# Kernel tuning notes

Measured on AMD Instinct MI355X. Metric: run time of the kernel, lower is better.

The kernel has to match this reference:

```python
import jax, jax.numpy as jnp
import numpy as np

C = 256      # all_channel
HW = 60      # all_dim
D = HW * HW  # 3600 spatial tokens
B = 1        # batch (torch loop returns only the last sample)
ROUNDS = 5   # propagate_layers


def _attention(ex, q, W_lin, W_gate):
    # ex, q: [B,C,H,W]
    b = ex.shape[0]
    exf = ex.reshape(b, C, D)            # [b,C,D]
    qf = q.reshape(b, C, D)              # [b,C,D]
    # linear_e on exemplar tokens: y = x @ W^T  (torch Linear, no bias)
    corr = jnp.einsum('bdc,ec->bde', exf.transpose(0, 2, 1), W_lin)  # [b,D,C]
    A = jnp.einsum('bdc,bcj->bdj', corr, qf)  # [b,D,D] affinity
    # torch: B = softmax(A^T, dim=1); att = bmm(qf, B)
    # equivalent: att[b,c,i] = sum_j softmax_j(A[b,i,:])[j] * qf[b,c,j]
    P = jax.nn.softmax(A, axis=-1)            # [b,D,D]
    att = jnp.einsum('bij,bcj->bci', P, qf).reshape(b, C, HW, HW)
    # 1x1 conv gate (out channels = 1, no bias) + sigmoid
    mask = jax.nn.sigmoid(jnp.einsum('c,bchw->bhw', W_gate, att))[:, None]
    return att * mask


def _conv3x3(x, W, b):
    y = jax.lax.conv_general_dilated(
        x, W, window_strides=(1, 1), padding='SAME',
        dimension_numbers=('NCHW', 'OIHW', 'NCHW'))
    return y + b[None, :, None, None]


def _conv1x1(x, W, b):
    return jnp.einsum('oi,bihw->bohw', W, x) + b[None, :, None, None]


def _convgru(inp, prev, Wr, br, Wu, bu, Wo, bo):
    st = jnp.concatenate([inp, prev], axis=1)                 # [b,2C,H,W]
    u = jax.nn.sigmoid(_conv1x1(st, Wu, bu))                  # update gate
    r = jax.nn.sigmoid(_conv1x1(st, Wr, br))                  # reset gate
    o = jnp.tanh(_conv1x1(jnp.concatenate([inp, prev * r], axis=1), Wo, bo))
    return prev * (1.0 - u) + o * u


def setup_inputs() -> dict:
    key = jax.random.key(0)
    ks = jax.random.split(key, 10)
    f32 = jnp.float32
    g = lambda k, shape, s: jax.random.normal(k, shape, dtype=f32) * s
    return {
        'infeature1': jax.random.normal(ks[0], (B, C, HW, HW), f32),
        'infeature2': jax.random.normal(ks[1], (B, C, HW, HW), f32),
        'infeature3': jax.random.normal(ks[2], (B, C, HW, HW), f32),
        'W_lin': g(ks[3], (C, C), 0.02),          # linear_e weight [out,in]
        'W_gate': g(ks[4], (C,), 0.01),           # gate 1x1 conv (out=1)
        'W_cf': g(ks[5], (C, 2 * C, 3, 3), 0.01), # conv_fusion OIHW
        'b_cf': jnp.zeros((C,), f32),
        'W_reset': g(ks[6], (C, 2 * C), 0.02), 'b_reset': jnp.zeros((C,), f32),
        'W_update': g(ks[7], (C, 2 * C), 0.02), 'b_update': jnp.zeros((C,), f32),
        'W_out': g(ks[8], (C, 2 * C), 0.02), 'b_out': jnp.zeros((C,), f32),
    }


def reference(infeature1, infeature2, infeature3, W_lin, W_gate, W_cf, b_cf,
              W_reset, b_reset, W_update, b_update, W_out, b_out):
    ex, q, q1 = infeature1, infeature2, infeature3
    for _ in range(ROUNDS):
        a1 = _conv3x3(jnp.concatenate([_attention(ex, q, W_lin, W_gate),
                                       _attention(ex, q1, W_lin, W_gate)], 1), W_cf, b_cf)
        a2 = _conv3x3(jnp.concatenate([_attention(q, ex, W_lin, W_gate),
                                       _attention(q, q1, W_lin, W_gate)], 1), W_cf, b_cf)
        a3 = _conv3x3(jnp.concatenate([_attention(q1, ex, W_lin, W_gate),
                                       _attention(q1, q, W_lin, W_gate)], 1), W_cf, b_cf)
        h1 = _convgru(a1, ex, W_reset, b_reset, W_update, b_update, W_out, b_out)
        h2 = _convgru(a2, q, W_reset, b_reset, W_update, b_update, W_out, b_out)
        h3 = _convgru(a3, q1, W_reset, b_reset, W_update, b_update, W_out, b_out)
        ex, q, q1 = h1, h2, h3
    # torch forward returns the exemplar/query/query1 of the LAST batch sample
    return (ex[-1:], q[-1:], q1[-1:])
```

## Files before the change

kernel.cpp:

```cpp
#include <hip/hip_runtime.h>

typedef float f32x4_t __attribute__((ext_vector_type(4)));
typedef short bf16x8_t __attribute__((ext_vector_type(8)));

#define MFMA16(A,B,C) __builtin_amdgcn_mfma_f32_16x16x32_bf16((A),(B),(C),0,0,0)

static constexpr int CC = 256;
static constexpr int NP = 3600;
static constexpr int PP = 3648;
static constexpr int CPOS = 3906;

static constexpr size_t SZ_F  = (size_t)PP*CC*4;
static constexpr size_t SZ_H  = (size_t)PP*CC*2;
static constexpr size_t SZ_CV = (size_t)CPOS*512*2;

static constexpr size_t O_SF   = 0;
static constexpr size_t O_STH  = O_SF   + 3*SZ_F;
static constexpr size_t O_STL  = O_STH  + 3*SZ_H;
static constexpr size_t O_SCH  = O_STL  + 3*SZ_H;
static constexpr size_t O_SCL  = O_SCH  + 3*SZ_H;
static constexpr size_t O_CORH = O_SCL  + 3*SZ_H;
static constexpr size_t O_CORL = O_CORH + 3*SZ_H;
static constexpr size_t O_CVH  = O_CORL + 3*SZ_H;
static constexpr size_t O_CVL  = O_CVH  + 3*SZ_CV;
static constexpr size_t O_WLH  = O_CVL  + 3*SZ_CV;
static constexpr size_t O_WLL  = O_WLH  + 131072;
static constexpr size_t O_WURH = O_WLL  + 131072;
static constexpr size_t O_WURL = O_WURH + 524288;
static constexpr size_t O_WOH  = O_WURL + 524288;
static constexpr size_t O_WOL  = O_WOH  + 262144;
static constexpr size_t O_WKH  = O_WOL  + 262144;
static constexpr size_t O_WKL  = O_WKH  + 2359296;
static constexpr size_t O_X    = O_WKL  + 2359296;
static constexpr size_t O_PML  = O_X;
static constexpr size_t O_PO   = O_X + 1048576;
static constexpr size_t O_AH   = O_X;
static constexpr size_t O_AL   = O_AH + 3*SZ_H;
static constexpr size_t O_U    = O_AL + 3*SZ_H;
static constexpr size_t O_PRH  = O_U  + 3*SZ_F;
static constexpr size_t O_PRL  = O_PRH + 3*SZ_H;

#define WSPTR(T, OFF) ((T*)(ws + (OFF)))

__device__ __forceinline__ unsigned short f2bf(float f){
  unsigned u = __builtin_bit_cast(unsigned, f);
  u += 0x7FFFu + ((u >> 16) & 1u);
  return (unsigned short)(u >> 16);
}
__device__ __forceinline__ float bf2f(unsigned short h){
  unsigned u = ((unsigned)h) << 16;
  return __builtin_bit_cast(float, u);
}
__device__ __forceinline__ void split_bf(float x, unsigned short &h, unsigned short &l){
  h = f2bf(x);
  l = f2bf(x - bf2f(h));
}

__device__ __forceinline__ void gll16(const void* g, void* l){
  __builtin_amdgcn_global_load_lds(
      (const __attribute__((address_space(1))) unsigned*)g,
      (__attribute__((address_space(3))) unsigned*)l, 16, 0, 0);
}

__device__ __forceinline__ void stage64(unsigned short* dst, const unsigned short* __restrict__ src, int ld){
  int t = threadIdx.x, r0 = t >> 3, c8 = (t & 7) * 8;
  #pragma unroll
  for(int h = 0; h < 2; h++){
    int r = r0 + h*32;
    *(bf16x8_t*)&dst[r*72 + c8] = *(const bf16x8_t*)&src[(size_t)r*ld + c8];
  }
}

__device__ __forceinline__ void mfma64(const unsigned short* Ah, const unsigned short* Al,
                                       const unsigned short* Bh, const unsigned short* Bl,
                                       f32x4_t acc[4], int lane, int wid){
  int kb = (lane >> 4) * 8, lr = lane & 15;
  int arow = wid*16 + lr;
  #pragma unroll
  for(int kk = 0; kk < 2; kk++){
    bf16x8_t ah = *(const bf16x8_t*)&Ah[arow*72 + kk*32 + kb];
    bf16x8_t al = *(const bf16x8_t*)&Al[arow*72 + kk*32 + kb];
    #pragma unroll
    for(int ct = 0; ct < 4; ct++){
      int brow = ct*16 + lr;
      bf16x8_t bh = *(const bf16x8_t*)&Bh[brow*72 + kk*32 + kb];
      bf16x8_t bl = *(const bf16x8_t*)&Bl[brow*72 + kk*32 + kb];
      acc[ct] = MFMA16(ah, bh, acc[ct]);
      acc[ct] = MFMA16(ah, bl, acc[ct]);
      acc[ct] = MFMA16(al, bh, acc[ct]);
    }
  }
}

__global__ void k_zero(char* ws){
  size_t n = (6*SZ_CV)/16;
  uint4* p = (uint4*)(ws + O_CVH);
  uint4 z = {0,0,0,0};
  for(size_t x = (size_t)blockIdx.x*256 + threadIdx.x; x < n; x += (size_t)gridDim.x*256) p[x] = z;
}

__global__ void k_weights(char* ws, const float* __restrict__ Wlin, const float* __restrict__ Wup,
                          const float* __restrict__ Wrs, const float* __restrict__ Wo,
                          const float* __restrict__ Wcf){
  const size_t N1 = 65536, N2 = N1 + 262144, N3 = N2 + 131072, N4 = N3 + 1179648;
  for(size_t x = (size_t)blockIdx.x*256 + threadIdx.x; x < N4; x += (size_t)gridDim.x*256){
    float v; unsigned short *dh, *dl; size_t off;
    if(x < N1){
      v = Wlin[x]; dh = WSPTR(unsigned short, O_WLH); dl = WSPTR(unsigned short, O_WLL); off = x;
    } else if(x < N2){
      size_t i = x - N1; int e = (int)(i >> 9), c = (int)(i & 511);
      v = (e < 256) ? Wup[(size_t)e*512 + c] : Wrs[(size_t)(e-256)*512 + c];
      dh = WSPTR(unsigned short, O_WURH); dl = WSPTR(unsigned short, O_WURL); off = i;
    } else if(x < N3){
      size_t i = x - N2; v = Wo[i];
      dh = WSPTR(unsigned short, O_WOH); dl = WSPTR(unsigned short, O_WOL); off = i;
    } else {
      size_t i = x - N3; int t = (int)(i % 9); size_t rest = i / 9;
      int ic = (int)(rest & 511), o = (int)(rest >> 9);
      v = Wcf[i]; off = (size_t)t*131072 + (size_t)o*512 + ic;
      dh = WSPTR(unsigned short, O_WKH); dl = WSPTR(unsigned short, O_WKL);
    }
    unsigned short h, l; split_bf(v, h, l);
    dh[off] = h; dl[off] = l;
  }
}

__global__ __launch_bounds__(256) void k_transpose(char* ws, const float* __restrict__ in0,
                                                   const float* __restrict__ in1, const float* __restrict__ in2){
  __shared__ float tile[64*65];
  int z = blockIdx.z;
  const float* in = z == 0 ? in0 : (z == 1 ? in1 : in2);
  int p0 = blockIdx.x*64, c0 = blockIdx.y*64;
  float* sF = WSPTR(float, O_SF) + (size_t)z*PP*CC;
  unsigned short* sTh = WSPTR(unsigned short, O_STH) + (size_t)z*PP*CC;
  unsigned short* sTl = WSPTR(unsigned short, O_STL) + (size_t)z*PP*CC;
  unsigned short* sCh = WSPTR(unsigned short, O_SCH) + (size_t)z*PP*CC;
  unsigned short* sCl = WSPTR(unsigned short, O_SCL) + (size_t)z*PP*CC;
  int t = threadIdx.x, pl = t & 63, cq = t >> 6;
  #pragma unroll
  for(int rr = 0; rr < 16; rr++){
    int cl = rr*4 + cq, p = p0 + pl, c = c0 + cl;
    float v = (p < NP) ? in[(size_t)c*NP + p] : 0.f;
    tile[cl*65 + pl] = v;
    if(p < NP){
      unsigned short h, l; split_bf(v, h, l);
      sCh[(size_t)c*PP + p] = h; sCl[(size_t)c*PP + p] = l;
    }
  }
  __syncthreads();
  #pragma unroll
  for(int rr = 0; rr < 16; rr++){
    int prow = rr*4 + cq, p = p0 + prow, cl = pl;
    if(p < NP){
      float v = tile[cl*65 + prow];
      int c = c0 + cl;
      sF[(size_t)p*CC + c] = v;
      unsigned short h, l; split_bf(v, h, l);
      sTh[(size_t)p*CC + c] = h; sTl[(size_t)p*CC + c] = l;
    }
  }
}

__global__ __launch_bounds__(256,4) void k_corr(char* ws){
  __shared__ unsigned short Ah[64*72], Al[64*72], Bh[64*72], Bl[64*72];
  int z = blockIdx.z, m0 = blockIdx.x*64, n0 = blockIdx.y*64;
  const unsigned short* aH = WSPTR(const unsigned short, O_STH) + (size_t)z*PP*CC;
  const unsigned short* aL = WSPTR(const unsigned short, O_STL) + (size_t)z*PP*CC;
  const unsigned short* bH = WSPTR(const unsigned short, O_WLH);
  const unsigned short* bL = WSPTR(const unsigned short, O_WLL);
  unsigned short* cH = WSPTR(unsigned short, O_CORH) + (size_t)z*PP*CC;
  unsigned short* cL = WSPTR(unsigned short, O_CORL) + (size_t)z*PP*CC;
  int lane = threadIdx.x & 63, wid = threadIdx.x >> 6;
  f32x4_t acc[4] = {};
  for(int k0 = 0; k0 < 256; k0 += 64){
    __syncthreads();
    stage64(Ah, aH + (size_t)m0*256 + k0, 256);
    stage64(Al, aL + (size_t)m0*256 + k0, 256);
    stage64(Bh, bH + (size_t)n0*256 + k0, 256);
    stage64(Bl, bL + (size_t)n0*256 + k0, 256);
    __syncthreads();
    mfma64(Ah, Al, Bh, Bl, acc, lane, wid);
  }
  #pragma unroll
  for(int r = 0; r < 4; r++){
    int i = m0 + wid*16 + (lane >> 4)*4 + r;
    if(i >= NP) continue;
    #pragma unroll
    for(int ct = 0; ct < 4; ct++){
      int c = n0 + ct*16 + (lane & 15);
      unsigned short h, l; split_bf(acc[ct][r], h, l);
      cH[(size_t)i*CC + c] = h; cL[(size_t)i*CC + c] = l;
    }
  }
}

__global__ __launch_bounds__(256,2) void k_flash(char* ws, int nspl){
  __shared__ unsigned short KV[32768];
  __shared__ unsigned short PBh[4][1024], PBl[4][1024];
  int qt = blockIdx.x, pair = blockIdx.y, sp = blockIdx.z;
  int src = pair >> 1;
  int tgt = ((pair & 1) == 0) ? (src == 0 ? 1 : 0) : (src == 2 ? 1 : 2);
  const unsigned short* Qh = WSPTR(const unsigned short, O_CORH) + (size_t)src*PP*CC;
  const unsigned short* Ql = WSPTR(const unsigned short, O_CORL) + (size_t)src*PP*CC;
  const unsigned short* Kh = WSPTR(const unsigned short, O_STH)  + (size_t)tgt*PP*CC;
  const unsigned short* Kl = WSPTR(const unsigned short, O_STL)  + (size_t)tgt*PP*CC;
  const unsigned short* Vh = WSPTR(const unsigned short, O_SCH)  + (size_t)tgt*PP*CC;
  const unsigned short* Vl = WSPTR(const unsigned short, O_SCL)  + (size_t)tgt*PP*CC;
  int t = threadIdx.x, lane = t & 63, wid = t >> 6, lr = lane & 15, lk = lane >> 4;
  int rowi = lane >> 5, c_lds = lane & 31;
  int vrow8 = lane >> 3, vj = lane & 7;

  #pragma unroll
  for(int q = 0; q < 8; q++){
    int n = wid*8 + q;
    int row = 2*n + rowi;
    int gch = c_lds ^ (row & 7);
    size_t ga = (size_t)(qt*64 + row)*256 + gch*8;
    gll16(&Qh[ga], &KV[n*512]);
    gll16(&Ql[ga], &KV[16384 + n*512]);
  }
  asm volatile("s_waitcnt vmcnt(0)" ::: "memory");
  __syncthreads();
  bf16x8_t qh[8], ql[8];
  {
    int qr = wid*16 + lr;
    #pragma unroll
    for(int kq = 0; kq < 8; kq++){
      int ch = (kq*4 + lk) ^ (lr & 7);
      qh[kq] = *(const bf16x8_t*)&KV[qr*256 + ch*8];
      ql[kq] = *(const bf16x8_t*)&KV[16384 + qr*256 + ch*8];
    }
  }
  __syncthreads();

  float m = -1e38f, lsum = 0.f;
  f32x4_t oacc[16] = {};
  int kt0 = (57*sp)/nspl, kt1 = (57*(sp+1))/nspl;

  for(int kt = kt0; kt < kt1; kt++){
    int j0 = kt*64;
    #pragma unroll
    for(int q = 0; q < 8; q++){
      int n = wid*8 + q;
      int row = 2*n + rowi;
      int gch = c_lds ^ (row & 7);
      size_t ga = (size_t)(j0 + row)*256 + gch*8;
      gll16(&Kh[ga], &KV[n*512]);
      gll16(&Kl[ga], &KV[16384 + n*512]);
    }
    asm volatile("s_waitcnt vmcnt(0)" ::: "memory");
    __syncthreads();
    f32x4_t s[4] = {};
    __builtin_amdgcn_s_setprio(1);
    #pragma unroll
    for(int kq = 0; kq < 8; kq++){
      #pragma unroll
      for(int ct = 0; ct < 4; ct++){
        int row = ct*16 + lr;
        int ch = (kq*4 + lk) ^ (lr & 7);
        bf16x8_t khv = *(const bf16x8_t*)&KV[row*256 + ch*8];
        bf16x8_t klv = *(const bf16x8_t*)&KV[16384 + row*256 + ch*8];
        s[ct] = MFMA16(khv, qh[kq], s[ct]);
        s[ct] = MFMA16(khv, ql[kq], s[ct]);
        s[ct] = MFMA16(klv, qh[kq], s[ct]);
      }
    }
    __builtin_amdgcn_s_setprio(0);
    if(kt == 56){
      #pragma unroll
      for(int ct = 1; ct < 4; ct++){ s[ct][0] = -1e30f; s[ct][1] = -1e30f; s[ct][2] = -1e30f; s[ct][3] = -1e30f; }
    }
    float pmax = s[0][0];
    #pragma unroll
    for(int ct = 0; ct < 4; ct++){
      #pragma unroll
      for(int r = 0; r < 4; r++) pmax = fmaxf(pmax, s[ct][r]);
    }
    pmax = fmaxf(pmax, __shfl_xor(pmax, 16));
    pmax = fmaxf(pmax, __shfl_xor(pmax, 32));
    bool need = pmax > m + 8.f;
    if(__any(need)){
      float mn = need ? pmax : m;
      float sc = __expf(m - mn);
      lsum *= sc;
      #pragma unroll
      for(int c = 0; c < 16; c++){ oacc[c][0]*=sc; oacc[c][1]*=sc; oacc[c][2]*=sc; oacc[c][3]*=sc; }
      m = mn;
    }
    float ps = 0.f;
    float pv[16];
    #pragma unroll
    for(int ct = 0; ct < 4; ct++){
      pv[ct*4+0] = __expf(s[ct][0]-m); pv[ct*4+1] = __expf(s[ct][1]-m);
      pv[ct*4+2] = __expf(s[ct][2]-m); pv[ct*4+3] = __expf(s[ct][3]-m);
      ps += (pv[ct*4+0]+pv[ct*4+1]) + (pv[ct*4+2]+pv[ct*4+3]);
    }
    ps += __shfl_xor(ps, 16);
    ps += __shfl_xor(ps, 32);
    lsum += ps;
    __syncthreads();
    #pragma unroll
    for(int q = 0; q < 8; q++){
      int n = wid*8 + q;
      int row = 8*n + vrow8;
      int gch = vj ^ (row & 7);
      size_t ga = (size_t)row*PP + j0 + gch*8;
      gll16(&Vh[ga], &KV[n*512]);
      gll16(&Vl[ga], &KV[16384 + n*512]);
    }
    #pragma unroll
    for(int ct = 0; ct < 4; ct++){
      unsigned short h0,l0,h1,l1,h2,l2,h3,l3;
      split_bf(pv[ct*4+0],h0,l0); split_bf(pv[ct*4+1],h1,l1);
      split_bf(pv[ct*4+2],h2,l2); split_bf(pv[ct*4+3],h3,l3);
      int chunk = ct*2 + (lk>>1);
      int idx = lr*64 + ((chunk ^ (lr&7))*8) + (lk&1)*4;
      uint2 wh = { (unsigned)h0 | ((unsigned)h1<<16), (unsigned)h2 | ((unsigned)h3<<16) };
      uint2 wl = { (unsigned)l0 | ((unsigned)l1<<16), (unsigned)l2 | ((unsigned)l3<<16) };
      *(uint2*)&PBh[wid][idx] = wh;
      *(uint2*)&PBl[wid][idx] = wl;
    }
    asm volatile("s_waitcnt vmcnt(0)" ::: "memory");
    __syncthreads();
    __builtin_amdgcn_s_setprio(1);
    #pragma unroll
    for(int kk = 0; kk < 2; kk++){
      int pidx = lr*64 + (((kk*4+lk) ^ (lr&7))*8);
      bf16x8_t pah = *(const bf16x8_t*)&PBh[wid][pidx];
      bf16x8_t pal = *(const bf16x8_t*)&PBl[wid][pidx];
      #pragma unroll
      for(int c16 = 0; c16 < 16; c16++){
        int c = c16*16 + lr;
        int ch = (kk*4 + lk) ^ (lr & 7);
        bf16x8_t vh  = *(const bf16x8_t*)&KV[c*64 + ch*8];
        bf16x8_t vlo = *(const bf16x8_t*)&KV[16384 + c*64 + ch*8];
        oacc[c16] = MFMA16(vh,  pah, oacc[c16]);
        oacc[c16] = MFMA16(vh,  pal, oacc[c16]);
        oacc[c16] = MFMA16(vlo, pah, oacc[c16]);
      }
    }
    __builtin_amdgcn_s_setprio(0);
    __syncthreads();
  }
  int idx = (pair*57 + qt)*nspl + sp;
  float* pml = WSPTR(float, O_PML) + (size_t)idx*128;
  float* po  = WSPTR(float, O_PO)  + (size_t)idx*16384;
  int il = wid*16 + lr;
  if(lk == 0){ pml[il] = m; pml[64 + il] = lsum; }
  #pragma unroll
  for(int c16 = 0; c16 < 16; c16++){
    *(f32x4_t*)&po[(size_t)il*256 + c16*16 + lk*4] = oacc[c16];
  }
}

__global__ __launch_bounds__(256) void k_merge(char* ws, const float* __restrict__ wgate, int nspl){
  int qt = blockIdx.x, pair = blockIdx.y;
  int src = pair >> 1, cho = (pair & 1)*256;
  unsigned short* cvH = WSPTR(unsigned short, O_CVH) + (size_t)src*CPOS*512 + cho;
  unsigned short* cvL = WSPTR(unsigned short, O_CVL) + (size_t)src*CPOS*512 + cho;
  int t = threadIdx.x, il = t >> 2, q4 = t & 3;
  int base = (pair*57 + qt)*nspl;
  const float* pml = WSPTR(const float, O_PML);
  const float* po  = WSPTR(const float, O_PO);
  float M = -1e38f;
  for(int s = 0; s < nspl; s++) M = fmaxf(M, pml[(size_t)(base+s)*128 + il]);
  float L = 0.f;
  float acc[64];
  #pragma unroll
  for(int k = 0; k < 64; k++) acc[k] = 0.f;
  for(int s = 0; s < nspl; s++){
    float w = __expf(pml[(size_t)(base+s)*128 + il] - M);
    L += pml[(size_t)(base+s)*128 + 64 + il]*w;
    const float* p = &po[(size_t)(base+s)*16384 + (size_t)il*256];
    #pragma unroll
    for(int k4 = 0; k4 < 16; k4++){
      f32x4_t v = *(const f32x4_t*)&p[k4*16 + q4*4];
      acc[k4*4+0] += v[0]*w; acc[k4*4+1] += v[1]*w;
      acc[k4*4+2] += v[2]*w; acc[k4*4+3] += v[3]*w;
    }
  }
  float invL = 1.f/L, g = 0.f;
  #pragma unroll
  for(int k4 = 0; k4 < 16; k4++){
    #pragma unroll
    for(int e = 0; e < 4; e++){
      acc[k4*4+e] *= invL;
      g += wgate[k4*16 + q4*4 + e] * acc[k4*4+e];
    }
  }
  g += __shfl_xor(g, 1);
  g += __shfl_xor(g, 2);
  g = 1.f/(1.f + __expf(-g));
  int i = qt*64 + il;
  if(i < NP){
    int pos = (1 + i/60)*62 + 1 + i%60;
    #pragma unroll
    for(int k4 = 0; k4 < 16; k4++){
      unsigned short h0,l0,h1,l1,h2,l2,h3,l3;
      split_bf(acc[k4*4+0]*g, h0, l0); split_bf(acc[k4*4+1]*g, h1, l1);
      split_bf(acc[k4*4+2]*g, h2, l2); split_bf(acc[k4*4+3]*g, h3, l3);
      uint2 wh = { (unsigned)h0 | ((unsigned)h1<<16), (unsigned)h2 | ((unsigned)h3<<16) };
      uint2 wl = { (unsigned)l0 | ((unsigned)l1<<16), (unsigned)l2 | ((unsigned)l3<<16) };
      *(uint2*)&cvH[(size_t)pos*512 + k4*16 + q4*4] = wh;
      *(uint2*)&cvL[(size_t)pos*512 + k4*16 + q4*4] = wl;
    }
  }
}

__global__ __launch_bounds__(256,4) void k_conv(char* ws, const float* __restrict__ bcf){
  __shared__ unsigned short Ah[64*72], Al[64*72], Bh[64*72], Bl[64*72];
  int z = blockIdx.z, y = blockIdx.x, n0 = blockIdx.y*64;
  const unsigned short* cvH = WSPTR(const unsigned short, O_CVH) + (size_t)z*CPOS*512;
  const unsigned short* cvL = WSPTR(const unsigned short, O_CVL) + (size_t)z*CPOS*512;
  const unsigned short* wH = WSPTR(const unsigned short, O_WKH);
  const unsigned short* wL = WSPTR(const unsigned short, O_WKL);
  unsigned short* oH = WSPTR(unsigned short, O_AH) + (size_t)z*PP*CC;
  unsigned short* oL = WSPTR(unsigned short, O_AL) + (size_t)z*PP*CC;
  int lane = threadIdx.x & 63, wid = threadIdx.x >> 6;
  f32x4_t acc[4] = {};
  for(int t = 0; t < 9; t++){
    int posBase = (y + t/3)*62 + (t%3);
    const unsigned short* aH = cvH + (size_t)posBase*512;
    const unsigned short* aL = cvL + (size_t)posBase*512;
    const unsigned short* bH = wH + (size_t)t*131072 + (size_t)n0*512;
    const unsigned short* bL = wL + (size_t)t*131072 + (size_t)n0*512;
    for(int k0 = 0; k0 < 512; k0 += 64){
      __syncthreads();
      stage64(Ah, aH + k0, 512);
      stage64(Al, aL + k0, 512);
      stage64(Bh, bH + k0, 512);
      stage64(Bl, bL + k0, 512);
      __syncthreads();
      mfma64(Ah, Al, Bh, Bl, acc, lane, wid);
    }
  }
  #pragma unroll
  for(int r = 0; r < 4; r++){
    int x = wid*16 + (lane >> 4)*4 + r;
    if(x >= 60) continue;
    int i = y*60 + x;
    #pragma unroll
    for(int ct = 0; ct < 4; ct++){
      int c = n0 + ct*16 + (lane & 15);
      float v = acc[ct][r] + bcf[c];
      unsigned short h, l; split_bf(v, h, l);
      oH[(size_t)i*CC + c] = h; oL[(size_t)i*CC + c] = l;
    }
  }
}

__global__ __launch_bounds__(256,4) void k_gates(char* ws, const float* __restrict__ bu, const float* __restrict__ br){
  __shared__ unsigned short Ah[64*72], Al[64*72], Bh[64*72], Bl[64*72];
  int z = blockIdx.z, m0 = blockIdx.x*64, n0 = blockIdx.y*64;
  const unsigned short* aH0 = WSPTR(const unsigned short, O_AH)  + (size_t)z*PP*CC;
  const unsigned short* aL0 = WSPTR(const unsigned short, O_AL)  + (size_t)z*PP*CC;
  const unsigned short* aH1 = WSPTR(const unsigned short, O_STH) + (size_t)z*PP*CC;
  const unsigned short* aL1 = WSPTR(const unsigned short, O_STL) + (size_t)z*PP*CC;
  const unsigned short* bH  = WSPTR(const unsigned short, O_WURH) + (size_t)n0*512;
  const unsigned short* bL  = WSPTR(const unsigned short, O_WURL) + (size_t)n0*512;
  const float* prevF = WSPTR(const float, O_SF) + (size_t)z*PP*CC;
  float* uOut = WSPTR(float, O_U) + (size_t)z*PP*CC;
  unsigned short* prH = WSPTR(unsigned short, O_PRH) + (size_t)z*PP*CC;
  unsigned short* prL = WSPTR(unsigned short, O_PRL) + (size_t)z*PP*CC;
  int lane = threadIdx.x & 63, wid = threadIdx.x >> 6;
  f32x4_t acc[4] = {};
  for(int ks = 0; ks < 8; ks++){
    const unsigned short* sah = (ks < 4) ? aH0 : aH1;
    const unsigned short* sal = (ks < 4) ? aL0 : aL1;
    int koff = (ks & 3) * 64;
    __syncthreads();
    stage64(Ah, sah + (size_t)m0*256 + koff, 256);
    stage64(Al, sal + (size_t)m0*256 + koff, 256);
    stage64(Bh, bH + ks*64, 512);
    stage64(Bl, bL + ks*64, 512);
    __syncthreads();
    mfma64(Ah, Al, Bh, Bl, acc, lane, wid);
  }
  #pragma unroll
  for(int r = 0; r < 4; r++){
    int i = m0 + wid*16 + (lane >> 4)*4 + r;
    if(i >= NP) continue;
    #pragma unroll
    for(int ct = 0; ct < 4; ct++){
      int c = n0 + ct*16 + (lane & 15);
      float pre = acc[ct][r] + (c < 256 ? bu[c] : br[c - 256]);
      float sg = 1.f / (1.f + __expf(-pre));
      if(c < 256){
        uOut[(size_t)i*CC + c] = sg;
      } else {
        int e = c - 256;
        float pv = prevF[(size_t)i*CC + e];
        unsigned short h, l; split_bf(sg * pv, h, l);
        prH[(size_t)i*CC + e] = h; prL[(size_t)i*CC + e] = l;
      }
    }
  }
}

__global__ __launch_bounds__(256,4) void k_gruo(char* ws, const float* __restrict__ bo, float* __restrict__ dout, int fin){
  __shared__ unsigned short Ah[64*72], Al[64*72], Bh[64*72], Bl[64*72];
  int z = blockIdx.z, m0 = blockIdx.x*64, n0 = blockIdx.y*64;
  const unsigned short* aH0 = WSPTR(const unsigned short, O_AH)  + (size_t)z*PP*CC;
  const unsigned short* aL0 = WSPTR(const unsigned short, O_AL)  + (size_t)z*PP*CC;
  const unsigned short* aH1 = WSPTR(const unsigned short, O_PRH) + (size_t)z*PP*CC;
  const unsigned short* aL1 = WSPTR(const unsigned short, O_PRL) + (size_t)z*PP*CC;
  const unsigned short* bH  = WSPTR(const unsigned short, O_WOH) + (size_t)n0*512;
  const unsigned short* bL  = WSPTR(const unsigned short, O_WOL) + (size_t)n0*512;
  const float* uBuf = WSPTR(const float, O_U) + (size_t)z*PP*CC;
  float* sF = WSPTR(float, O_SF) + (size_t)z*PP*CC;
  unsigned short* sTh = WSPTR(unsigned short, O_STH) + (size_t)z*PP*CC;
  unsigned short* sTl = WSPTR(unsigned short, O_STL) + (size_t)z*PP*CC;
  unsigned short* sCh = WSPTR(unsigned short, O_SCH) + (size_t)z*PP*CC;
  unsigned short* sCl = WSPTR(unsigned short, O_SCL) + (size_t)z*PP*CC;
  int lane = threadIdx.x & 63, wid = threadIdx.x >> 6;
  f32x4_t acc[4] = {};
  for(int ks = 0; ks < 8; ks++){
    const unsigned short* sah = (ks < 4) ? aH0 : aH1;
    const unsigned short* sal = (ks < 4) ? aL0 : aL1;
    int koff = (ks & 3) * 64;
    __syncthreads();
    stage64(Ah, sah + (size_t)m0*256 + koff, 256);
    stage64(Al, sal + (size_t)m0*256 + koff, 256);
    stage64(Bh, bH + ks*64, 512);
    stage64(Bl, bL + ks*64, 512);
    __syncthreads();
    mfma64(Ah, Al, Bh, Bl, acc, lane, wid);
  }
  #pragma unroll
  for(int r = 0; r < 4; r++){
    int i = m0 + wid*16 + (lane >> 4)*4 + r;
    if(i >= NP) continue;
    #pragma unroll
    for(int ct = 0; ct < 4; ct++){
      int c = n0 + ct*16 + (lane & 15);
      float o = tanhf(acc[ct][r] + bo[c]);
      float uu = uBuf[(size_t)i*CC + c];
      float pv = sF[(size_t)i*CC + c];
      float h = pv*(1.f - uu) + o*uu;
      if(fin){
        dout[(size_t)z*921600 + (size_t)c*3600 + i] = h;
      } else {
        sF[(size_t)i*CC + c] = h;
        unsigned short hh, hl; split_bf(h, hh, hl);
        sTh[(size_t)i*CC + c] = hh; sTl[(size_t)i*CC + c] = hl;
        sCh[(size_t)c*PP + i] = hh; sCl[(size_t)c*PP + i] = hl;
      }
    }
  }
}

extern "C" void kernel_launch(void* const* d_in, const int* in_sizes, int n_in,
                              void* d_out, int out_size, void* d_ws, size_t ws_size,
                              hipStream_t stream){
  char* ws = (char*)d_ws;
  const float* in1   = (const float*)d_in[0];
  const float* in2   = (const float*)d_in[1];
  const float* in3   = (const float*)d_in[2];
  const float* Wlin  = (const float*)d_in[3];
  const float* Wgate = (const float*)d_in[4];
  const float* Wcf   = (const float*)d_in[5];
  const float* bcf   = (const float*)d_in[6];
  const float* Wr    = (const float*)d_in[7];
  const float* br_   = (const float*)d_in[8];
  const float* Wu    = (const float*)d_in[9];
  const float* bu_   = (const float*)d_in[10];
  const float* Wo    = (const float*)d_in[11];
  const float* bo_   = (const float*)d_in[12];

  int nspl = 3;
  while(nspl > 1 && O_PO + (size_t)342*nspl*65536 > ws_size) nspl--;

  k_zero<<<dim3(2048), dim3(256), 0, stream>>>(ws);
  k_weights<<<dim3(1024), dim3(256), 0, stream>>>(ws, Wlin, Wu, Wr, Wo, Wcf);
  k_transpose<<<dim3(57, 4, 3), dim3(256), 0, stream>>>(ws, in1, in2, in3);

  for(int rd = 0; rd < 5; rd++){
    k_corr <<<dim3(57, 4, 3), dim3(256), 0, stream>>>(ws);
    k_flash<<<dim3(57, 6, nspl), dim3(256), 0, stream>>>(ws, nspl);
    k_merge<<<dim3(57, 6), dim3(256), 0, stream>>>(ws, Wgate, nspl);
    k_conv <<<dim3(60, 4, 3), dim3(256), 0, stream>>>(ws, bcf);
    k_gates<<<dim3(57, 8, 3), dim3(256), 0, stream>>>(ws, bu_, br_);
    k_gruo <<<dim3(57, 4, 3), dim3(256), 0, stream>>>(ws, bo_, (float*)d_out, rd == 4 ? 1 : 0);
  }
}
```

Measured before the change: 2.737 ms.

## Restructure flash attention: 128-query blocks, double-buffered K, register P, XCD-aware scheduling

Each flash workgroup grows to 512 threads covering 128 query rows, so every K/V tile loaded into LDS is shared by twice as many queries. The K tile for the next step is prefetched into a second LDS buffer while the current step's QK MFMAs run. The probability tile no longer goes through an LDS staging buffer; it is rearranged into MFMA operand layout with lane shuffles and the PV product swaps operand order to match. Blocks are launched on a 1D grid and remapped so neighbouring work lands on the same XCD, and the split count rises to 4. Merge and workspace layout are adjusted to match. The costs are a larger LDS footprint (64K shorts), more shuffle traffic, and a bigger partial-output buffer.

```diff
diff --git a/kernel.cpp b/kernel.cpp
--- a/kernel.cpp
+++ b/kernel.cpp
@@ -33,7 +33,7 @@
 static constexpr size_t O_WKL  = O_WKH  + 2359296;
 static constexpr size_t O_X    = O_WKL  + 2359296;
 static constexpr size_t O_PML  = O_X;
-static constexpr size_t O_PO   = O_X + 1048576;
+static constexpr size_t O_PO   = O_X + 2097152;
 static constexpr size_t O_AH   = O_X;
 static constexpr size_t O_AL   = O_AH + 3*SZ_H;
 static constexpr size_t O_U    = O_AL + 3*SZ_H;
@@ -194,10 +194,12 @@
   }
 }
 
-__global__ __launch_bounds__(256,2) void k_flash(char* ws, int nspl){
-  __shared__ unsigned short KV[32768];
-  __shared__ unsigned short PBh[4][1024], PBl[4][1024];
-  int qt = blockIdx.x, pair = blockIdx.y, sp = blockIdx.z;
+__global__ __launch_bounds__(512,2) void k_flash(char* ws, int nspl){
+  __shared__ unsigned short KV[65536];
+  int n_wg = 174*nspl, lin = blockIdx.x;
+  int qq = n_wg >> 3, rr = n_wg & 7, xcd = lin & 7, pos = lin >> 3;
+  int wg = (xcd < rr ? xcd*(qq+1) : rr*(qq+1) + (xcd-rr)*qq) + pos;
+  int qt = wg % 29, pair = (wg / 29) % 6, sp = wg / 174;
   int src = pair >> 1;
   int tgt = ((pair & 1) == 0) ? (src == 0 ? 1 : 0) : (src == 2 ? 1 : 2);
   const unsigned short* Qh = WSPTR(const unsigned short, O_CORH) + (size_t)src*PP*CC;
@@ -207,28 +209,28 @@
   const unsigned short* Vh = WSPTR(const unsigned short, O_SCH)  + (size_t)tgt*PP*CC;
   const unsigned short* Vl = WSPTR(const unsigned short, O_SCL)  + (size_t)tgt*PP*CC;
   int t = threadIdx.x, lane = t & 63, wid = t >> 6, lr = lane & 15, lk = lane >> 4;
-  int rowi = lane >> 5, c_lds = lane & 31;
-  int vrow8 = lane >> 3, vj = lane & 7;
 
   #pragma unroll
   for(int q = 0; q < 8; q++){
     int n = wid*8 + q;
-    int row = 2*n + rowi;
-    int gch = c_lds ^ (row & 7);
-    size_t ga = (size_t)(qt*64 + row)*256 + gch*8;
-    gll16(&Qh[ga], &KV[n*512]);
-    gll16(&Ql[ga], &KV[16384 + n*512]);
+    int row = 2*n + (lane >> 5);
+    int gch = (lane & 31) ^ (row & 7);
+    size_t ga = (size_t)(qt*128 + row)*256 + gch*8;
+    unsigned short* d = &KV[(row >> 6)*32768 + (n & 31)*512];
+    gll16(&Qh[ga], d);
+    gll16(&Ql[ga], d + 16384);
   }
   asm volatile("s_waitcnt vmcnt(0)" ::: "memory");
   __syncthreads();
   bf16x8_t qh[8], ql[8];
   {
-    int qr = wid*16 + lr;
+    int qbase = (wid >> 2)*32768;
+    int qrow = (wid & 3)*16 + lr;
     #pragma unroll
     for(int kq = 0; kq < 8; kq++){
       int ch = (kq*4 + lk) ^ (lr & 7);
-      qh[kq] = *(const bf16x8_t*)&KV[qr*256 + ch*8];
-      ql[kq] = *(const bf16x8_t*)&KV[16384 + qr*256 + ch*8];
+      qh[kq] = *(const bf16x8_t*)&KV[qbase + qrow*256 + ch*8];
+      ql[kq] = *(const bf16x8_t*)&KV[qbase + 16384 + qrow*256 + ch*8];
     }
   }
   __syncthreads();
@@ -236,36 +238,67 @@
   float m = -1e38f, lsum = 0.f;
   f32x4_t oacc[16] = {};
   int kt0 = (57*sp)/nspl, kt1 = (57*(sp+1))/nspl;
+  int cur = 0;
+
+  {
+    int j0 = kt0*64;
+    #pragma unroll
+    for(int q = 0; q < 4; q++){
+      int n = wid*4 + q;
+      int row = 2*n + (lane >> 5);
+      int gch = (lane & 31) ^ (row & 7);
+      size_t ga = (size_t)(j0 + row)*256 + gch*8;
+      unsigned short* d = &KV[n*512];
+      gll16(&Kh[ga], d);
+      gll16(&Kl[ga], d + 16384);
+    }
+  }
 
   for(int kt = kt0; kt < kt1; kt++){
     int j0 = kt*64;
-    #pragma unroll
-    for(int q = 0; q < 8; q++){
-      int n = wid*8 + q;
-      int row = 2*n + rowi;
-      int gch = c_lds ^ (row & 7);
-      size_t ga = (size_t)(j0 + row)*256 + gch*8;
-      gll16(&Kh[ga], &KV[n*512]);
-      gll16(&Kl[ga], &KV[16384 + n*512]);
-    }
     asm volatile("s_waitcnt vmcnt(0)" ::: "memory");
     __syncthreads();
+    if(kt + 1 < kt1){
+      int j1 = (kt+1)*64;
+      #pragma unroll
+      for(int q = 0; q < 4; q++){
+        int n = wid*4 + q;
+        int row = 2*n + (lane >> 5);
+        int gch = (lane & 31) ^ (row & 7);
+        size_t ga = (size_t)(j1 + row)*256 + gch*8;
+        unsigned short* d = &KV[(cur^1)*32768 + n*512];
+        gll16(&Kh[ga], d);
+        gll16(&Kl[ga], d + 16384);
+      }
+    }
+    const unsigned short* Kb = &KV[cur*32768];
     f32x4_t s[4] = {};
     __builtin_amdgcn_s_setprio(1);
     #pragma unroll
     for(int kq = 0; kq < 8; kq++){
       #pragma unroll
       for(int ct = 0; ct < 4; ct++){
-        int row = ct*16 + lr;
+        int arow = ct*16 + lr;
         int ch = (kq*4 + lk) ^ (lr & 7);
-        bf16x8_t khv = *(const bf16x8_t*)&KV[row*256 + ch*8];
-        bf16x8_t klv = *(const bf16x8_t*)&KV[16384 + row*256 + ch*8];
+        bf16x8_t khv = *(const bf16x8_t*)&Kb[arow*256 + ch*8];
+        bf16x8_t klv = *(const bf16x8_t*)&Kb[16384 + arow*256 + ch*8];
         s[ct] = MFMA16(khv, qh[kq], s[ct]);
         s[ct] = MFMA16(khv, ql[kq], s[ct]);
         s[ct] = MFMA16(klv, qh[kq], s[ct]);
       }
     }
     __builtin_amdgcn_s_setprio(0);
+    __syncthreads();
+    #pragma unroll
+    for(int q = 0; q < 4; q++){
+      int n = wid*4 + q;
+      int c = 8*n + (lane >> 3);
+      int gch = (lane & 7) ^ (c & 7);
+      size_t ga = (size_t)c*PP + j0 + gch*8;
+      unsigned short* d = &KV[cur*32768 + n*512];
+      gll16(&Vh[ga], d);
+      gll16(&Vl[ga], d + 16384);
+    }
     if(kt == 56){
       #pragma unroll
       for(int ct = 1; ct < 4; ct++){ s[ct][0] = -1e30f; s[ct][1] = -1e30f; s[ct][2] = -1e30f; s[ct][3] = -1e30f; }
@@ -282,10 +315,14 @@
     if(__any(need)){
       float mn = need ? pmax : m;
       float sc = __expf(m - mn);
-      lsum *= sc;
-      #pragma unroll
-      for(int c = 0; c < 16; c++){ oacc[c][0]*=sc; oacc[c][1]*=sc; oacc[c][2]*=sc; oacc[c][3]*=sc; }
-      m = mn;
+      m = mn; lsum *= sc;
+      float sc4[4];
+      #pragma unroll
+      for(int r = 0; r < 4; r++) sc4[r] = __shfl(sc, 4*lk + r);
+      #pragma unroll
+      for(int c = 0; c < 16; c++){
+        oacc[c][0]*=sc4[0]; oacc[c][1]*=sc4[1]; oacc[c][2]*=sc4[2]; oacc[c][3]*=sc4[3];
+      }
     }
     float ps = 0.f;
     float pv[16];
@@ -298,80 +335,76 @@
     ps += __shfl_xor(ps, 16);
     ps += __shfl_xor(ps, 32);
     lsum += ps;
-    __syncthreads();
-    #pragma unroll
-    for(int q = 0; q < 8; q++){
-      int n = wid*8 + q;
-      int row = 8*n + vrow8;
-      int gch = vj ^ (row & 7);
-      size_t ga = (size_t)row*PP + j0 + gch*8;
-      gll16(&Vh[ga], &KV[n*512]);
-      gll16(&Vl[ga], &KV[16384 + n*512]);
-    }
-    #pragma unroll
-    for(int ct = 0; ct < 4; ct++){
-      unsigned short h0,l0,h1,l1,h2,l2,h3,l3;
-      split_bf(pv[ct*4+0],h0,l0); split_bf(pv[ct*4+1],h1,l1);
-      split_bf(pv[ct*4+2],h2,l2); split_bf(pv[ct*4+3],h3,l3);
-      int chunk = ct*2 + (lk>>1);
-      int idx = lr*64 + ((chunk ^ (lr&7))*8) + (lk&1)*4;
-      uint2 wh = { (unsigned)h0 | ((unsigned)h1<<16), (unsigned)h2 | ((unsigned)h3<<16) };
-      uint2 wl = { (unsigned)l0 | ((unsigned)l1<<16), (unsigned)l2 | ((unsigned)l3<<16) };
-      *(uint2*)&PBh[wid][idx] = wh;
-      *(uint2*)&PBl[wid][idx] = wl;
+    bf16x8_t pah[2], pal[2];
+    #pragma unroll
+    for(int kk = 0; kk < 2; kk++){
+      #pragma unroll
+      for(int ri = 0; ri < 4; ri++){
+        int srcA = lr + 16*((2*lk) & 3);
+        int srcB = lr + 16*((2*lk + 1) & 3);
+        float a0 = __shfl(pv[(2*kk)*4 + ri],   srcA);
+        float a1 = __shfl(pv[(2*kk+1)*4 + ri], srcA);
+        float b0 = __shfl(pv[(2*kk)*4 + ri],   srcB);
+        float b1 = __shfl(pv[(2*kk+1)*4 + ri], srcB);
+        float va = (lk < 2) ? a0 : a1;
+        float vb = (lk < 2) ? b0 : b1;
+        unsigned short h, l;
+        split_bf(va, h, l); pah[kk][ri]   = (short)h; pal[kk][ri]   = (short)l;
+        split_bf(vb, h, l); pah[kk][4+ri] = (short)h; pal[kk][4+ri] = (short)l;
+      }
     }
     asm volatile("s_waitcnt vmcnt(0)" ::: "memory");
     __syncthreads();
+    const unsigned short* Vb = &KV[cur*32768];
     __builtin_amdgcn_s_setprio(1);
     #pragma unroll
     for(int kk = 0; kk < 2; kk++){
-      int pidx = lr*64 + (((kk*4+lk) ^ (lr&7))*8);
-      bf16x8_t pah = *(const bf16x8_t*)&PBh[wid][pidx];
-      bf16x8_t pal = *(const bf16x8_t*)&PBl[wid][pidx];
       #pragma unroll
       for(int c16 = 0; c16 < 16; c16++){
-        int c = c16*16 + lr;
+        int crow = c16*16 + lr;
         int ch = (kk*4 + lk) ^ (lr & 7);
-        bf16x8_t vh  = *(const bf16x8_t*)&KV[c*64 + ch*8];
-        bf16x8_t vlo = *(const bf16x8_t*)&KV[16384 + c*64 + ch*8];
-        oacc[c16] = MFMA16(vh,  pah, oacc[c16]);
-        oacc[c16] = MFMA16(vh,  pal, oacc[c16]);
-        oacc[c16] = MFMA16(vlo, pah, oacc[c16]);
+        bf16x8_t vh  = *(const bf16x8_t*)&Vb[crow*64 + ch*8];
+        bf16x8_t vlo = *(const bf16x8_t*)&Vb[16384 + crow*64 + ch*8];
+        oacc[c16] = MFMA16(pah[kk], vh,  oacc[c16]);
+        oacc[c16] = MFMA16(pah[kk], vlo, oacc[c16]);
+        oacc[c16] = MFMA16(pal[kk], vh,  oacc[c16]);
       }
     }
     __builtin_amdgcn_s_setprio(0);
-    __syncthreads();
-  }
-  int idx = (pair*57 + qt)*nspl + sp;
-  float* pml = WSPTR(float, O_PML) + (size_t)idx*128;
-  float* po  = WSPTR(float, O_PO)  + (size_t)idx*16384;
-  int il = wid*16 + lr;
-  if(lk == 0){ pml[il] = m; pml[64 + il] = lsum; }
+    cur ^= 1;
+  }
+  int idx = (pair*29 + qt)*nspl + sp;
+  float* pml = WSPTR(float, O_PML) + (size_t)idx*256;
+  float* po  = WSPTR(float, O_PO)  + (size_t)idx*32768;
+  if(lk == 0){ pml[wid*16 + lr] = m; pml[128 + wid*16 + lr] = lsum; }
   #pragma unroll
   for(int c16 = 0; c16 < 16; c16++){
-    *(f32x4_t*)&po[(size_t)il*256 + c16*16 + lk*4] = oacc[c16];
-  }
-}
-
-__global__ __launch_bounds__(256) void k_merge(char* ws, const float* __restrict__ wgate, int nspl){
+    #pragma unroll
+    for(int r = 0; r < 4; r++){
+      po[(size_t)(wid*16 + 4*lk + r)*256 + c16*16 + lr] = oacc[c16][r];
+    }
+  }
+}
+
+__global__ __launch_bounds__(512) void k_merge(char* ws, const float* __restrict__ wgate, int nspl){
   int qt = blockIdx.x, pair = blockIdx.y;
   int src = pair >> 1, cho = (pair & 1)*256;
   unsigned short* cvH = WSPTR(unsigned short, O_CVH) + (size_t)src*CPOS*512 + cho;
   unsigned short* cvL = WSPTR(unsigned short, O_CVL) + (size_t)src*CPOS*512 + cho;
   int t = threadIdx.x, il = t >> 2, q4 = t & 3;
-  int base = (pair*57 + qt)*nspl;
+  int base = (pair*29 + qt)*nspl;
   const float* pml = WSPTR(const float, O_PML);
   const float* po  = WSPTR(const float, O_PO);
   float M = -1e38f;
-  for(int s = 0; s < nspl; s++) M = fmaxf(M, pml[(size_t)(base+s)*128 + il]);
+  for(int s = 0; s < nspl; s++) M = fmaxf(M, pml[(size_t)(base+s)*256 + il]);
   float L = 0.f;
   float acc[64];
   #pragma unroll
   for(int k = 0; k < 64; k++) acc[k] = 0.f;
   for(int s = 0; s < nspl; s++){
-    float w = __expf(pml[(size_t)(base+s)*128 + il] - M);
-    L += pml[(size_t)(base+s)*128 + 64 + il]*w;
-    const float* p = &po[(size_t)(base+s)*16384 + (size_t)il*256];
+    float w = __expf(pml[(size_t)(base+s)*256 + il] - M);
+    L += pml[(size_t)(base+s)*256 + 128 + il]*w;
+    const float* p = &po[(size_t)(base+s)*32768 + (size_t)il*256];
     #pragma unroll
     for(int k4 = 0; k4 < 16; k4++){
       f32x4_t v = *(const f32x4_t*)&p[k4*16 + q4*4];
@@ -391,7 +424,7 @@
   g += __shfl_xor(g, 1);
   g += __shfl_xor(g, 2);
   g = 1.f/(1.f + __expf(-g));
-  int i = qt*64 + il;
+  int i = qt*128 + il;
   if(i < NP){
     int pos = (1 + i/60)*62 + 1 + i%60;
     #pragma unroll
@@ -567,8 +600,8 @@
   const float* Wo    = (const float*)d_in[11];
   const float* bo_   = (const float*)d_in[12];
 
-  int nspl = 3;
-  while(nspl > 1 && O_PO + (size_t)342*nspl*65536 > ws_size) nspl--;
+  int nspl = 4;
+  while(nspl > 1 && O_PO + (size_t)174*nspl*131072 > ws_size) nspl--;
 
   k_zero<<<dim3(2048), dim3(256), 0, stream>>>(ws);
   k_weights<<<dim3(1024), dim3(256), 0, stream>>>(ws, Wlin, Wu, Wr, Wo, Wcf);
@@ -576,8 +609,8 @@
 
   for(int rd = 0; rd < 5; rd++){
     k_corr <<<dim3(57, 4, 3), dim3(256), 0, stream>>>(ws);
-    k_flash<<<dim3(57, 6, nspl), dim3(256), 0, stream>>>(ws, nspl);
-    k_merge<<<dim3(57, 6), dim3(256), 0, stream>>>(ws, Wgate, nspl);
+    k_flash<<<dim3(174*nspl), dim3(512), 0, stream>>>(ws, nspl);
+    k_merge<<<dim3(29, 6), dim3(512), 0, stream>>>(ws, Wgate, nspl);
     k_conv <<<dim3(60, 4, 3), dim3(256), 0, stream>>>(ws, bcf);
     k_gates<<<dim3(57, 8, 3), dim3(256), 0, stream>>>(ws, bu_, br_);
     k_gruo <<<dim3(57, 4, 3), dim3(256), 0, stream>>>(ws, bo_, (float*)d_out, rd == 4 ? 1 : 0);
```

New measurement: 2.638 ms. 1.04x faster.

## Pipeline K/V loads in flash kernel, keep P in registers, remap blocks per XCD

Applied to the files above, without the earlier changes.

The flash-attention kernel now prefetches the next K tile at the end of each iteration. It issues the V tile load right after the QK MFMAs, so the memory traffic overlaps the softmax work. The probability tile is packed to bf16 with v_cvt_pk_bf16_f32 and moved between lanes with shuffles instead of a round trip through shared memory. The low-order bf16 part of P is dropped, which cuts the PV MFMAs from three to two per step at some accuracy cost. The flash and conv grids are flattened and remapped so neighbouring work-groups land on the same XCD for better L2 reuse, and the output store is rewritten for the transposed accumulator layout.

```diff
diff --git a/kernel.cpp b/kernel.cpp
--- a/kernel.cpp
+++ b/kernel.cpp
@@ -33,7 +33,7 @@
 static constexpr size_t O_WKL  = O_WKH  + 2359296;
 static constexpr size_t O_X    = O_WKL  + 2359296;
 static constexpr size_t O_PML  = O_X;
-static constexpr size_t O_PO   = O_X + 1048576;
+static constexpr size_t O_PO   = O_X + 2097152;
 static constexpr size_t O_AH   = O_X;
 static constexpr size_t O_AL   = O_AH + 3*SZ_H;
 static constexpr size_t O_U    = O_AL + 3*SZ_H;
@@ -196,8 +196,10 @@
 
 __global__ __launch_bounds__(256,2) void k_flash(char* ws, int nspl){
   __shared__ unsigned short KV[32768];
-  __shared__ unsigned short PBh[4][1024], PBl[4][1024];
-  int qt = blockIdx.x, pair = blockIdx.y, sp = blockIdx.z;
+  int n_wg = 342*nspl, lin = blockIdx.x;
+  int qq = n_wg >> 3, rr2 = n_wg & 7, xcd = lin & 7, pos = lin >> 3;
+  int wg = (xcd < rr2 ? xcd*(qq+1) : rr2*(qq+1) + (xcd-rr2)*qq) + pos;
+  int qt = wg % 57, sp = (wg/57) % nspl, pair = wg/(57*nspl);
   int src = pair >> 1;
   int tgt = ((pair & 1) == 0) ? (src == 0 ? 1 : 0) : (src == 2 ? 1 : 2);
   const unsigned short* Qh = WSPTR(const unsigned short, O_CORH) + (size_t)src*PP*CC;
@@ -207,14 +209,12 @@
   const unsigned short* Vh = WSPTR(const unsigned short, O_SCH)  + (size_t)tgt*PP*CC;
   const unsigned short* Vl = WSPTR(const unsigned short, O_SCL)  + (size_t)tgt*PP*CC;
   int t = threadIdx.x, lane = t & 63, wid = t >> 6, lr = lane & 15, lk = lane >> 4;
-  int rowi = lane >> 5, c_lds = lane & 31;
-  int vrow8 = lane >> 3, vj = lane & 7;
 
   #pragma unroll
   for(int q = 0; q < 8; q++){
     int n = wid*8 + q;
-    int row = 2*n + rowi;
-    int gch = c_lds ^ (row & 7);
+    int row = 2*n + (lane >> 5);
+    int gch = (lane & 31) ^ (row & 7);
     size_t ga = (size_t)(qt*64 + row)*256 + gch*8;
     gll16(&Qh[ga], &KV[n*512]);
     gll16(&Ql[ga], &KV[16384 + n*512]);
@@ -223,12 +223,12 @@
   __syncthreads();
   bf16x8_t qh[8], ql[8];
   {
-    int qr = wid*16 + lr;
+    int qrow = wid*16 + lr;
     #pragma unroll
     for(int kq = 0; kq < 8; kq++){
       int ch = (kq*4 + lk) ^ (lr & 7);
-      qh[kq] = *(const bf16x8_t*)&KV[qr*256 + ch*8];
-      ql[kq] = *(const bf16x8_t*)&KV[16384 + qr*256 + ch*8];
+      qh[kq] = *(const bf16x8_t*)&KV[qrow*256 + ch*8];
+      ql[kq] = *(const bf16x8_t*)&KV[16384 + qrow*256 + ch*8];
     }
   }
   __syncthreads();
@@ -237,17 +237,18 @@
   f32x4_t oacc[16] = {};
   int kt0 = (57*sp)/nspl, kt1 = (57*(sp+1))/nspl;
 
+  #pragma unroll
+  for(int q = 0; q < 8; q++){
+    int n = wid*8 + q;
+    int row = 2*n + (lane >> 5);
+    int gch = (lane & 31) ^ (row & 7);
+    size_t ga = (size_t)(kt0*64 + row)*256 + gch*8;
+    gll16(&Kh[ga], &KV[n*512]);
+    gll16(&Kl[ga], &KV[16384 + n*512]);
+  }
+
   for(int kt = kt0; kt < kt1; kt++){
     int j0 = kt*64;
-    #pragma unroll
-    for(int q = 0; q < 8; q++){
-      int n = wid*8 + q;
-      int row = 2*n + rowi;
-      int gch = c_lds ^ (row & 7);
-      size_t ga = (size_t)(j0 + row)*256 + gch*8;
-      gll16(&Kh[ga], &KV[n*512]);
-      gll16(&Kl[ga], &KV[16384 + n*512]);
-    }
     asm volatile("s_waitcnt vmcnt(0)" ::: "memory");
     __syncthreads();
     f32x4_t s[4] = {};
@@ -256,16 +257,26 @@
     for(int kq = 0; kq < 8; kq++){
       #pragma unroll
       for(int ct = 0; ct < 4; ct++){
-        int row = ct*16 + lr;
+        int arow = ct*16 + lr;
         int ch = (kq*4 + lk) ^ (lr & 7);
-        bf16x8_t khv = *(const bf16x8_t*)&KV[row*256 + ch*8];
-        bf16x8_t klv = *(const bf16x8_t*)&KV[16384 + row*256 + ch*8];
+        bf16x8_t khv = *(const bf16x8_t*)&KV[arow*256 + ch*8];
+        bf16x8_t klv = *(const bf16x8_t*)&KV[16384 + arow*256 + ch*8];
         s[ct] = MFMA16(khv, qh[kq], s[ct]);
         s[ct] = MFMA16(khv, ql[kq], s[ct]);
         s[ct] = MFMA16(klv, qh[kq], s[ct]);
       }
     }
     __builtin_amdgcn_s_setprio(0);
+    __syncthreads();
+    #pragma unroll
+    for(int q = 0; q < 8; q++){
+      int n = wid*8 + q;
+      int c = 8*n + (lane >> 3);
+      int gch = (lane & 7) ^ (c & 7);
+      size_t ga = (size_t)c*PP + j0 + gch*8;
+      gll16(&Vh[ga], &KV[n*512]);
+      gll16(&Vl[ga], &KV[16384 + n*512]);
+    }
     if(kt == 56){
       #pragma unroll
       for(int ct = 1; ct < 4; ct++){ s[ct][0] = -1e30f; s[ct][1] = -1e30f; s[ct][2] = -1e30f; s[ct][3] = -1e30f; }
@@ -282,10 +293,14 @@
     if(__any(need)){
       float mn = need ? pmax : m;
       float sc = __expf(m - mn);
-      lsum *= sc;
-      #pragma unroll
-      for(int c = 0; c < 16; c++){ oacc[c][0]*=sc; oacc[c][1]*=sc; oacc[c][2]*=sc; oacc[c][3]*=sc; }
-      m = mn;
+      m = mn; lsum *= sc;
+      float sc4[4];
+      #pragma unroll
+      for(int r = 0; r < 4; r++) sc4[r] = __shfl(sc, 4*lk + r);
+      #pragma unroll
+      for(int c = 0; c < 16; c++){
+        oacc[c][0]*=sc4[0]; oacc[c][1]*=sc4[1]; oacc[c][2]*=sc4[2]; oacc[c][3]*=sc4[3];
+      }
     }
     float ps = 0.f;
     float pv[16];
@@ -298,58 +313,69 @@
     ps += __shfl_xor(ps, 16);
     ps += __shfl_xor(ps, 32);
     lsum += ps;
-    __syncthreads();
-    #pragma unroll
-    for(int q = 0; q < 8; q++){
-      int n = wid*8 + q;
-      int row = 8*n + vrow8;
-      int gch = vj ^ (row & 7);
-      size_t ga = (size_t)row*PP + j0 + gch*8;
-      gll16(&Vh[ga], &KV[n*512]);
-      gll16(&Vl[ga], &KV[16384 + n*512]);
-    }
-    #pragma unroll
-    for(int ct = 0; ct < 4; ct++){
-      unsigned short h0,l0,h1,l1,h2,l2,h3,l3;
-      split_bf(pv[ct*4+0],h0,l0); split_bf(pv[ct*4+1],h1,l1);
-      split_bf(pv[ct*4+2],h2,l2); split_bf(pv[ct*4+3],h3,l3);
-      int chunk = ct*2 + (lk>>1);
-      int idx = lr*64 + ((chunk ^ (lr&7))*8) + (lk&1)*4;
-      uint2 wh = { (unsigned)h0 | ((unsigned)h1<<16), (unsigned)h2 | ((unsigned)h3<<16) };
-      uint2 wl = { (unsigned)l0 | ((unsigned)l1<<16), (unsigned)l2 | ((unsigned)l3<<16) };
-      *(uint2*)&PBh[wid][idx] = wh;
-      *(uint2*)&PBl[wid][idx] = wl;
+    unsigned pkd[8];
+    #pragma unroll
+    for(int a = 0; a < 2; a++){
+      #pragma unroll
+      for(int ri = 0; ri < 4; ri++){
+        asm("v_cvt_pk_bf16_f32 %0, %1, %2" : "=v"(pkd[a*4+ri]) : "v"(pv[(2*a)*4+ri]), "v"(pv[(2*a+1)*4+ri]));
+      }
+    }
+    int srcA = lr + 16*((2*lk) & 3);
+    int srcB = lr + 16*((2*lk + 1) & 3);
+    bf16x8_t pah[2];
+    #pragma unroll
+    for(int kk = 0; kk < 2; kk++){
+      #pragma unroll
+      for(int ri = 0; ri < 4; ri++){
+        unsigned ua = (unsigned)__shfl((int)pkd[kk*4+ri], srcA);
+        unsigned ub = (unsigned)__shfl((int)pkd[kk*4+ri], srcB);
+        unsigned va = (lk < 2) ? (ua & 0xffffu) : (ua >> 16);
+        unsigned vb = (lk < 2) ? (ub & 0xffffu) : (ub >> 16);
+        pah[kk][ri]   = (short)va;
+        pah[kk][4+ri] = (short)vb;
+      }
     }
     asm volatile("s_waitcnt vmcnt(0)" ::: "memory");
     __syncthreads();
     __builtin_amdgcn_s_setprio(1);
     #pragma unroll
     for(int kk = 0; kk < 2; kk++){
-      int pidx = lr*64 + (((kk*4+lk) ^ (lr&7))*8);
-      bf16x8_t pah = *(const bf16x8_t*)&PBh[wid][pidx];
-      bf16x8_t pal = *(const bf16x8_t*)&PBl[wid][pidx];
       #pragma unroll
       for(int c16 = 0; c16 < 16; c16++){
-        int c = c16*16 + lr;
+        int crow = c16*16 + lr;
         int ch = (kk*4 + lk) ^ (lr & 7);
-        bf16x8_t vh  = *(const bf16x8_t*)&KV[c*64 + ch*8];
-        bf16x8_t vlo = *(const bf16x8_t*)&KV[16384 + c*64 + ch*8];
-        oacc[c16] = MFMA16(vh,  pah, oacc[c16]);
-        oacc[c16] = MFMA16(vh,  pal, oacc[c16]);
-        oacc[c16] = MFMA16(vlo, pah, oacc[c16]);
+        bf16x8_t vh  = *(const bf16x8_t*)&KV[crow*64 + ch*8];
+        bf16x8_t vlo = *(const bf16x8_t*)&KV[16384 + crow*64 + ch*8];
+        oacc[c16] = MFMA16(pah[kk], vh,  oacc[c16]);
+        oacc[c16] = MFMA16(pah[kk], vlo, oacc[c16]);
       }
     }
     __builtin_amdgcn_s_setprio(0);
     __syncthreads();
+    if(kt + 1 < kt1){
+      int j1 = (kt+1)*64;
+      #pragma unroll
+      for(int q = 0; q < 8; q++){
+        int n = wid*8 + q;
+        int row = 2*n + (lane >> 5);
+        int gch = (lane & 31) ^ (row & 7);
+        size_t ga = (size_t)(j1 + row)*256 + gch*8;
+        gll16(&Kh[ga], &KV[n*512]);
+        gll16(&Kl[ga], &KV[16384 + n*512]);
+      }
+    }
   }
   int idx = (pair*57 + qt)*nspl + sp;
   float* pml = WSPTR(float, O_PML) + (size_t)idx*128;
   float* po  = WSPTR(float, O_PO)  + (size_t)idx*16384;
-  int il = wid*16 + lr;
-  if(lk == 0){ pml[il] = m; pml[64 + il] = lsum; }
+  if(lk == 0){ pml[wid*16 + lr] = m; pml[64 + wid*16 + lr] = lsum; }
   #pragma unroll
   for(int c16 = 0; c16 < 16; c16++){
-    *(f32x4_t*)&po[(size_t)il*256 + c16*16 + lk*4] = oacc[c16];
+    #pragma unroll
+    for(int r = 0; r < 4; r++){
+      po[(size_t)(wid*16 + 4*lk + r)*256 + c16*16 + lr] = oacc[c16][r];
+    }
   }
 }
 
@@ -409,7 +435,10 @@
 
 __global__ __launch_bounds__(256,4) void k_conv(char* ws, const float* __restrict__ bcf){
   __shared__ unsigned short Ah[64*72], Al[64*72], Bh[64*72], Bl[64*72];
-  int z = blockIdx.z, y = blockIdx.x, n0 = blockIdx.y*64;
+  int lin = blockIdx.x;
+  int wg = (lin & 7)*90 + (lin >> 3);
+  int y = wg % 60, zn = wg / 60;
+  int n0 = (zn & 3)*64, z = zn >> 2;
   const unsigned short* cvH = WSPTR(const unsigned short, O_CVH) + (size_t)z*CPOS*512;
   const unsigned short* cvL = WSPTR(const unsigned short, O_CVL) + (size_t)z*CPOS*512;
   const unsigned short* wH = WSPTR(const unsigned short, O_WKH);
@@ -576,9 +605,9 @@
 
   for(int rd = 0; rd < 5; rd++){
     k_corr <<<dim3(57, 4, 3), dim3(256), 0, stream>>>(ws);
-    k_flash<<<dim3(57, 6, nspl), dim3(256), 0, stream>>>(ws, nspl);
+    k_flash<<<dim3(342*nspl), dim3(256), 0, stream>>>(ws, nspl);
     k_merge<<<dim3(57, 6), dim3(256), 0, stream>>>(ws, Wgate, nspl);
-    k_conv <<<dim3(60, 4, 3), dim3(256), 0, stream>>>(ws, bcf);
+    k_conv <<<dim3(720), dim3(256), 0, stream>>>(ws, bcf);
     k_gates<<<dim3(57, 8, 3), dim3(256), 0, stream>>>(ws, bu_, br_);
     k_gruo <<<dim3(57, 4, 3), dim3(256), 0, stream>>>(ws, bo_, (float*)d_out, rd == 4 ? 1 : 0);
   }
```

New measurement: 2.613 ms. 4.5% less time.
